# Performance work log

Measured on AMD Instinct MI355X. Metric: run time of the kernel, lower is better.

The kernel has to match this reference:

```python
import jax, jax.numpy as jnp
import numpy as np
from jax import lax

BN_EPS = 1e-5


def _conv1d(h, w, b=None):
    # h: [B, Cin, L], w: [Cout, Cin, K], 'same' padding for odd K
    k = w.shape[-1]
    out = lax.conv_general_dilated(h, w, (1,), [(k // 2, k // 2)],
                                   dimension_numbers=('NCH', 'OIH', 'NCH'))
    if b is not None:
        out = out + b[None, :, None]
    return out


def _bn(h, gamma, beta):
    # eval-mode BatchNorm1d with running_mean=0, running_var=1
    return h * (gamma[None, :, None] / jnp.sqrt(1.0 + BN_EPS)) + beta[None, :, None]


def _encoder(h, cw, cb, rw, gammas, betas, aw, au):
    # h: [B, D, L] -> V: [B, C, F]
    t = jnp.tanh(_conv1d(h, cw, cb))
    t = _bn(t, gammas[0], betas[0])
    for i in range(rw.shape[0]):  # residual blocks
        t = jnp.tanh(_bn(_conv1d(t, rw[i]), gammas[i + 1], betas[i + 1]) + t)
    # label attention: w [A,F], u [C,A]
    Z = jnp.tanh(jnp.einsum('af,bfl->bal', aw, t))
    A = jax.nn.softmax(jnp.einsum('ca,bal->bcl', au, Z), axis=2)
    V = jnp.einsum('bfl,bcl->bcf', t, A)
    return V


def setup_inputs() -> dict:
    key = jax.random.key(0)
    ks = list(jax.random.split(key, 32))
    B, L, D, C, VOC, NE, N, E = 16, 4096, 256, 50, 50000, 20050, 512, 8192
    F, A, FFN = 100, 256, 128

    def rn(k, shape, s):
        return (jax.random.normal(k, shape, jnp.float32) * s).astype(jnp.float32)

    x = jax.random.randint(ks[0], (B, L), 0, VOC)
    attention_mask = jnp.ones((B, L), jnp.int32)
    nodes = jax.random.randint(ks[1], (B, N), 0, NE)
    src = jax.random.randint(ks[2], (B, E), 0, N)
    off = jax.random.randint(ks[3], (B, E), 1, N)
    dst = (src + off) % N  # guaranteed no self-loops
    edges = jnp.stack([src, dst], axis=1)  # [B, 2, E]

    inp = dict(x=x, attention_mask=attention_mask, nodes=nodes, edges=edges)
    inp['word_emb'] = rn(ks[4], (VOC, D), 0.02)
    inp['entity_emb'] = rn(ks[5], (NE, D), 0.02)
    i = 6
    for ksz in (3, 5, 9):
        inp[f'convw{ksz}'] = rn(ks[i], (F, D, ksz), (2.0 / (D * ksz)) ** 0.5); i += 1
        inp[f'convb{ksz}'] = jnp.zeros((F,), jnp.float32)
        inp[f'resw{ksz}'] = rn(ks[i], (2, F, F, ksz), (2.0 / (F * ksz)) ** 0.5); i += 1
    inp['bn_gamma'] = jnp.ones((3, 3, F), jnp.float32)
    inp['bn_beta'] = jnp.zeros((3, 3, F), jnp.float32)
    inp['attn_w'] = rn(ks[i], (3, A, F), 0.05); i += 1
    inp['attn_u'] = rn(ks[i], (3, C, A), 0.05); i += 1
    inp['gc1_w'] = rn(ks[i], (D, D), (1.0 / D) ** 0.5); i += 1
    inp['gc1_b'] = jnp.zeros((D,), jnp.float32)
    inp['gc2_w'] = rn(ks[i], (D, D), (1.0 / D) ** 0.5); i += 1
    inp['gc2_b'] = jnp.zeros((D,), jnp.float32)
    inp['fin1_w'] = rn(ks[i], (FFN, 3 * F + D), 0.05); i += 1
    inp['fin1_b'] = jnp.zeros((FFN,), jnp.float32)
    inp['fin2_w'] = rn(ks[i], (C, FFN), 0.05); i += 1
    inp['fin2_b'] = jnp.zeros((C,), jnp.float32)
    return inp


def reference(x, attention_mask, nodes, edges, word_emb, entity_emb,
              convw3, convb3, resw3, convw5, convb5, resw5, convw9, convb9, resw9,
              bn_gamma, bn_beta, attn_w, attn_u,
              gc1_w, gc1_b, gc2_w, gc2_b, fin1_w, fin1_b, fin2_w, fin2_b):
    C = fin2_b.shape[0]
    h = word_emb[x]                      # [B, L, D]
    h = jnp.transpose(h, (0, 2, 1))      # [B, D, L]

    Vs = []
    for i, (cw, cb, rw) in enumerate([(convw3, convb3, resw3),
                                      (convw5, convb5, resw5),
                                      (convw9, convb9, resw9)]):
        Vs.append(_encoder(h, cw, cb, rw, bn_gamma[i], bn_beta[i], attn_w[i], attn_u[i]))
    V = jnp.concatenate(Vs, axis=2)      # [B, C, 300]

    node_emb = entity_emb[nodes]         # [B, N, D]

    def per_graph(ne, ei):
        N = ne.shape[0]
        sl = jnp.arange(N)
        s = jnp.concatenate([ei[0], sl])  # GCNConv adds self-loops
        d = jnp.concatenate([ei[1], sl])
        deg = jax.ops.segment_sum(jnp.ones(s.shape[0], jnp.float32), d, num_segments=N)
        dinv = jnp.where(deg > 0, lax.rsqrt(deg), 0.0)
        norm = (dinv[s] * dinv[d])[:, None]

        def gconv(hh, W, b):
            return jax.ops.segment_sum((hh @ W.T)[s] * norm, d, num_segments=N) + b

        g = jax.nn.relu(gconv(ne, gc1_w, gc1_b))
        g = gconv(g, gc2_w, gc2_b)
        return g[:C]

    out_graphs = jax.vmap(per_graph)(node_emb, edges)  # [B, C, D]

    out = jnp.concatenate([out_graphs, V], axis=2)     # [B, C, D+300]
    hid = jax.nn.relu(jnp.einsum('bcf,hf->bch', out, fin1_w) + fin1_b)
    y_hat = jnp.sum(fin2_w[None] * hid, axis=2) + fin2_b  # [B, C]
    return y_hat
```

## Files before the change

### kernel.cpp

```cpp
#include <hip/hip_runtime.h>


#define CDIV(a,b) (((a)+(b)-1)/(b))

#define B_    16
#define L_    4096
#define D_    256
#define LP_   4112
#define POFF  8
#define F_    100
#define A_    256
#define C_    50
#define NN_   512
#define EE_   8192
#define ADJ_  8704
#define OC_   560

#define WFC1_STRIDE ((size_t)9*8*8*512)
#define WFRES_STRIDE ((size_t)9*4*8*512)
#define WFAW_STRIDE ((size_t)4*16*512)
#define WFAU_STRIDE ((size_t)8*4*512)

typedef unsigned short u16;
using short8  = __attribute__((ext_vector_type(8))) short;
using short4v = __attribute__((ext_vector_type(4))) short;
using f32x4   = __attribute__((ext_vector_type(4))) float;

__device__ __forceinline__ u16 f2b(float f){
    unsigned u = __float_as_uint(f);
    u += 0x7FFF + ((u >> 16) & 1);
    return (u16)(u >> 16);
}
__device__ __forceinline__ float b2f(u16 h){ return __uint_as_float(((unsigned)h) << 16); }

__global__ void fill_i_k(int* p, int n, int v){
    int i = blockIdx.x*256 + threadIdx.x; if (i < n) p[i] = v;
}
__global__ void zero_pads1_k(u16* p){
    int idx = blockIdx.x*256 + threadIdx.x;
    if (idx >= B_*16*128) return;
    int ch = idx & 127; int rest = idx >> 7;
    int pc = rest & 15; int b = rest >> 4;
    int col = (pc < 8) ? pc : (4096 + pc);
    p[((size_t)b*LP_ + col)*128 + ch] = 0;
}

__global__ __launch_bounds__(256) void embed1_k(const int* __restrict__ x,
                                                const float* __restrict__ emb,
                                                u16* __restrict__ hH){
    int b = blockIdx.y;
    int col = blockIdx.x*8 + (threadIdx.x >> 5);
    int cg  = (threadIdx.x & 31) * 8;
    size_t o = ((size_t)b*LP_ + col)*D_ + cg;
    int l = col - POFF;
    short8 h0;
    if (l < 0 || l >= L_){
        #pragma unroll
        for (int i = 0; i < 8; ++i) h0[i] = 0;
    } else {
        int tok = x[b*L_ + l];
        const float* s = emb + (size_t)tok*D_ + cg;
        #pragma unroll
        for (int i = 0; i < 8; ++i) h0[i] = (short)f2b(s[i]);
    }
    *(short8*)(hH + o) = h0;
}

__device__ __forceinline__ void pack_frag(const float* src, u16* dst,
                                          int M, int K, int kt, int nch, int MTtot, int idx){
    int i = idx & 7, lane = (idx >> 3) & 63, rest = idx >> 9;
    int mt = rest % MTtot, r2 = rest / MTtot;
    int cc = r2 % nch,  j = r2 / nch;
    int m  = mt*16 + (lane & 15);
    int ch = cc*32 + (lane >> 4)*8 + i;
    float v = (m < M && ch < K) ? src[((size_t)m*K + ch)*kt + j] : 0.f;
    dst[(size_t)rest*512 + lane*8 + i] = f2b(v);
}
__global__ void pack_conv1_k(const float* w3, const float* w5, const float* w9, u16* dst){
    int br = blockIdx.y;
    int k = (br == 0) ? 3 : (br == 1) ? 5 : 9;
    const float* s = (br == 0) ? w3 : (br == 1) ? w5 : w9;
    int idx = blockIdx.x*256 + threadIdx.x;
    if (idx < k*8*8*512) pack_frag(s, dst + (size_t)br*WFC1_STRIDE, F_, 256, k, 8, 8, idx);
}
__global__ void pack_res_k(const float* w3, const float* w5, const float* w9, u16* dst){
    int br = blockIdx.y, blk = blockIdx.z;
    int k = (br == 0) ? 3 : (br == 1) ? 5 : 9;
    const float* s = ((br == 0) ? w3 : (br == 1) ? w5 : w9) + (size_t)blk*F_*F_*k;
    int idx = blockIdx.x*256 + threadIdx.x;
    if (idx < k*4*8*512) pack_frag(s, dst + (size_t)(br*2 + blk)*WFRES_STRIDE, F_, F_, k, 4, 8, idx);
}
__global__ void pack_aw_k(const float* aw, u16* dst){
    int br = blockIdx.y;
    int idx = blockIdx.x*256 + threadIdx.x;
    if (idx < 4*16*512) pack_frag(aw + (size_t)br*A_*F_, dst + (size_t)br*WFAW_STRIDE, A_, F_, 1, 4, 16, idx);
}
__global__ void pack_au_k(const float* au, u16* dst){
    int br = blockIdx.y;
    int idx = blockIdx.x*256 + threadIdx.x;
    if (idx < 8*4*512) pack_frag(au + (size_t)br*C_*A_, dst + (size_t)br*WFAU_STRIDE, C_, A_, 1, 8, 4, idx);
}
__global__ void transpose_fin1_k(const float* __restrict__ src, float* __restrict__ dst){
    int idx = blockIdx.x*256 + threadIdx.x;
    if (idx >= OC_*128) return;
    int h = idx & 127, j = idx >> 7;
    dst[idx] = (j < 556) ? src[h*556 + j] : 0.f;
}

template<int KT, int MODE>
__global__ __launch_bounds__(256) void conv_mfma_k(
    const u16* __restrict__ in, int CHp_in, int nch,
    const u16* __restrict__ wf,
    const float* __restrict__ bias, const float* __restrict__ gamma,
    const float* __restrict__ beta,
    u16* __restrict__ out, u16* __restrict__ outT)
{
    __shared__ short sm[4352];
    const int tid = threadIdx.x, lane = tid & 63;
    const int w = tid >> 6, wm = w >> 1, wn = w & 1;
    const int q = lane >> 4, lr = lane & 15;
    const int n0 = blockIdx.x * 64;
    const int b  = blockIdx.y;
    const u16* inb = in + (size_t)b*LP_*CHp_in;

    f32x4 acc[4][2];
    #pragma unroll
    for (int t = 0; t < 4; ++t)
        #pragma unroll
        for (int n = 0; n < 2; ++n) acc[t][n] = (f32x4){0.f,0.f,0.f,0.f};

    for (int cc = 0; cc < nch; ++cc){
        for (int idx = tid; idx < 320; idx += 256){
            int col = idx >> 2, qq = idx & 3;
            *(short8*)(sm + col*40 + qq*8) =
                *(const short8*)(inb + (size_t)(n0 + col)*CHp_in + cc*32 + qq*8);
        }
        __syncthreads();
        const u16* fpb = wf + (size_t)(cc*8 + wm*4)*512 + lane*8;
        short8 Ac[4];
        #pragma unroll
        for (int t = 0; t < 4; ++t) Ac[t] = *(const short8*)(fpb + (size_t)t*512);
        #pragma unroll
        for (int j = 0; j < KT; ++j){
            short8 An[4];
            if (j + 1 < KT){
                const u16* fn = fpb + (size_t)(j+1)*nch*8*512;
                #pragma unroll
                for (int t = 0; t < 4; ++t) An[t] = *(const short8*)(fn + (size_t)t*512);
            }
            int sc0 = 8 - (KT >> 1) + j + wn*32 + lr;
            short8 Bv[2];
            #pragma unroll
            for (int n = 0; n < 2; ++n)
                Bv[n] = *(const short8*)(sm + (sc0 + n*16)*40 + q*8);
            #pragma unroll
            for (int t = 0; t < 4; ++t)
                #pragma unroll
                for (int n = 0; n < 2; ++n)
                    acc[t][n] = __builtin_amdgcn_mfma_f32_16x16x32_bf16(Ac[t], Bv[n], acc[t][n], 0,0,0);
            if (j + 1 < KT){
                #pragma unroll
                for (int t = 0; t < 4; ++t) Ac[t] = An[t];
            }
        }
        __syncthreads();
    }

    const float BNS = 0.9999950000374997f;
    for (int p = 0; p < 2; ++p){
        if (wn == p){
            #pragma unroll
            for (int t = 0; t < 4; ++t){
                #pragma unroll
                for (int n = 0; n < 2; ++n){
                    int mbase = wm*64 + t*16 + q*4;
                    int cl = n*16 + lr;
                    int colg = n0 + p*32 + cl;
                    float rsum[4] = {0.f,0.f,0.f,0.f};
                    if (MODE == 1){
                        size_t ro = ((size_t)b*LP_ + POFF + colg)*CHp_in + mbase;
                        short4v rh = *(const short4v*)(in + ro);
                        #pragma unroll
                        for (int r = 0; r < 4; ++r) rsum[r] = b2f((u16)rh[r]);
                    }
                    short4v hv;
                    #pragma unroll
                    for (int r = 0; r < 4; ++r){
                        int mm = mbase + r;
                        float a = acc[t][n][r];
                        float v;
                        if (MODE == 0){
                            float bi=0.f, s=0.f, be=0.f;
                            if (mm < F_){ bi = bias[mm]; s = gamma[mm]*BNS; be = beta[mm]; }
                            v = tanhf(a + bi)*s + be;
                        } else {
                            float s=0.f, be=0.f;
                            if (mm < F_){ s = gamma[mm]*BNS; be = beta[mm]; }
                            v = tanhf(fmaf(a, s, be) + rsum[r]);
                        }
                        hv[r] = (short)f2b(v);
                    }
                    *(short4v*)(sm + cl*136 + mbase) = hv;
                }
            }
        }
        __syncthreads();
        for (int idx = tid; idx < 512; idx += 256){
            int col = idx >> 4, q8 = idx & 15;
            short8 vv = *(const short8*)(sm + col*136 + q8*8);
            *(short8*)(out + ((size_t)b*LP_ + POFF + n0 + p*32 + col)*128 + q8*8) = vv;
        }
        if (outT){
            int f = tid & 127, half = tid >> 7;
            u16 vals[16];
            #pragma unroll
            for (int i = 0; i < 16; ++i) vals[i] = (u16)sm[(half*16 + i)*136 + f];
            short8 v0, v1;
            #pragma unroll
            for (int i = 0; i < 8; ++i){ v0[i] = (short)vals[i]; v1[i] = (short)vals[8+i]; }
            u16* dst = outT + ((size_t)b*128 + f)*L_ + n0 + p*32 + half*16;
            *(short8*)dst = v0;
            *(short8*)(dst + 8) = v1;
        }
        __syncthreads();
    }
}

__global__ __launch_bounds__(256) void attn_k(const u16* __restrict__ tpl,
                                              const u16* __restrict__ awf,
                                              const u16* __restrict__ auf,
                                              float* __restrict__ S){
    __shared__ short sm[17408];
    const int tid = threadIdx.x, lane = tid & 63;
    const int w = tid >> 6, wm = w >> 1, wn = w & 1;
    const int q = lane >> 4, lr = lane & 15;
    const int n0 = blockIdx.x * 128;
    const int b  = blockIdx.y;

    for (int idx = tid; idx < 2048; idx += 256){
        int col = idx >> 4, g = idx & 15;
        *(short8*)(sm + col*136 + g*8) =
            *(const short8*)(tpl + ((size_t)b*LP_ + POFF + n0 + col)*128 + g*8);
    }
    __syncthreads();

    f32x4 acc1[8][4];
    #pragma unroll
    for (int t = 0; t < 8; ++t)
        #pragma unroll
        for (int n = 0; n < 4; ++n) acc1[t][n] = (f32x4){0.f,0.f,0.f,0.f};
    for (int cc = 0; cc < 4; ++cc){
        short8 Af[8];
        const u16* fp = awf + (size_t)(cc*16 + wm*8)*512 + lane*8;
        #pragma unroll
        for (int t = 0; t < 8; ++t) Af[t] = *(const short8*)(fp + (size_t)t*512);
        short8 Bf[4];
        #pragma unroll
        for (int n = 0; n < 4; ++n)
            Bf[n] = *(const short8*)(sm + (wn*64 + n*16 + lr)*136 + cc*32 + q*8);
        #pragma unroll
        for (int t = 0; t < 8; ++t)
            #pragma unroll
            for (int n = 0; n < 4; ++n)
                acc1[t][n] = __builtin_amdgcn_mfma_f32_16x16x32_bf16(Af[t], Bf[n], acc1[t][n], 0,0,0);
    }
    __syncthreads();

    for (int p = 0; p < 2; ++p){
        if (wn == p){
            #pragma unroll
            for (int t = 0; t < 8; ++t){
                #pragma unroll
                for (int n = 0; n < 4; ++n){
                    int abase = wm*128 + t*16 + q*4;
                    int cl = n*16 + lr;
                    short4v zv;
                    #pragma unroll
                    for (int r = 0; r < 4; ++r) zv[r] = (short)f2b(tanhf(acc1[t][n][r]));
                    *(short4v*)(sm + cl*264 + abase) = zv;
                }
            }
        }
        __syncthreads();
        f32x4 acc2[4];
        #pragma unroll
        for (int t = 0; t < 4; ++t) acc2[t] = (f32x4){0.f,0.f,0.f,0.f};
        for (int cc = 0; cc < 8; ++cc){
            short8 Af2[4];
            const u16* fp2 = auf + (size_t)(cc*4)*512 + lane*8;
            #pragma unroll
            for (int t = 0; t < 4; ++t) Af2[t] = *(const short8*)(fp2 + (size_t)t*512);
            short8 Bf2 = *(const short8*)(sm + (w*16 + lr)*264 + cc*32 + q*8);
            #pragma unroll
            for (int t = 0; t < 4; ++t)
                acc2[t] = __builtin_amdgcn_mfma_f32_16x16x32_bf16(Af2[t], Bf2, acc2[t], 0,0,0);
        }
        #pragma unroll
        for (int t = 0; t < 4; ++t)
            #pragma unroll
            for (int r = 0; r < 4; ++r){
                int c = t*16 + q*4 + r;
                S[((size_t)b*64 + c)*L_ + n0 + p*64 + w*16 + lr] = acc2[t][r];
            }
        __syncthreads();
    }
}

__global__ __launch_bounds__(256) void softmax_k(float* __restrict__ S){
    int c = blockIdx.x, b = blockIdx.y, t = threadIdx.x;
    float* p = S + ((size_t)b*64 + c)*L_;
    __shared__ float sh[256];
    float mx = -1e30f;
    for (int j = t; j < L_; j += 256) mx = fmaxf(mx, p[j]);
    sh[t] = mx; __syncthreads();
    for (int o = 128; o > 0; o >>= 1){ if (t < o) sh[t] = fmaxf(sh[t], sh[t+o]); __syncthreads(); }
    float m = sh[0]; __syncthreads();
    float sum = 0.f;
    for (int j = t; j < L_; j += 256){ float e = expf(p[j] - m); p[j] = e; sum += e; }
    sh[t] = sum; __syncthreads();
    for (int o = 128; o > 0; o >>= 1){ if (t < o) sh[t] += sh[t+o]; __syncthreads(); }
    float inv = 1.0f / sh[0];
    for (int j = t; j < L_; j += 256) p[j] *= inv;
}

__global__ __launch_bounds__(256) void v_mfma_k(const u16* __restrict__ tT,
                                                const float* __restrict__ S,
                                                float* __restrict__ Vpart){
    int cx = blockIdx.x, b = blockIdx.y;
    int w = threadIdx.x >> 6, lane = threadIdx.x & 63;
    int q = lane >> 4, lr = lane & 15;
    int l0 = cx*128;
    f32x4 acc[7];
    #pragma unroll
    for (int mt = 0; mt < 7; ++mt) acc[mt] = (f32x4){0.f,0.f,0.f,0.f};
    const u16* tb = tT + (size_t)b*128*L_;
    const float* Sb = S + ((size_t)b*64 + w*16 + lr)*L_;
    #pragma unroll
    for (int kk = 0; kk < 4; ++kk){
        int l = l0 + kk*32 + q*8;
        float4 s0 = *(const float4*)(Sb + l);
        float4 s1 = *(const float4*)(Sb + l + 4);
        short8 Bf;
        Bf[0] = (short)f2b(s0.x); Bf[1] = (short)f2b(s0.y);
        Bf[2] = (short)f2b(s0.z); Bf[3] = (short)f2b(s0.w);
        Bf[4] = (short)f2b(s1.x); Bf[5] = (short)f2b(s1.y);
        Bf[6] = (short)f2b(s1.z); Bf[7] = (short)f2b(s1.w);
        #pragma unroll
        for (int mt = 0; mt < 7; ++mt){
            short8 Af = *(const short8*)(tb + (size_t)(mt*16 + lr)*L_ + l);
            acc[mt] = __builtin_amdgcn_mfma_f32_16x16x32_bf16(Af, Bf, acc[mt], 0,0,0);
        }
    }
    int c = w*16 + lr;
    if (c < C_){
        float* vp = Vpart + ((size_t)(b*64 + c)*32 + cx)*112;
        #pragma unroll
        for (int mt = 0; mt < 7; ++mt)
            *(f32x4*)(vp + mt*16 + q*4) = acc[mt];
    }
}

__global__ void reduce_v_k(const float* __restrict__ Vp, float* __restrict__ oc, int coloff){
    int idx = blockIdx.x*256 + threadIdx.x;
    if (idx >= B_*C_*F_) return;
    int f = idx % F_; int rest = idx / F_;
    int c = rest % C_; int b = rest / C_;
    const float* src = Vp + ((size_t)(b*64 + c)*32)*112 + f;
    float s = 0.f;
    #pragma unroll
    for (int cx = 0; cx < 32; ++cx) s += src[cx*112];
    oc[((size_t)b*C_ + c)*OC_ + 256 + coloff + f] = s;
}

__global__ void gather_nodes_k(const int* __restrict__ nodes, const float* __restrict__ emb,
                               float* __restrict__ ne){
    int idx = blockIdx.x*256 + threadIdx.x;
    if (idx >= B_*NN_*D_) return;
    int d = idx & 255, n = (idx >> 8) & 511, b = idx >> 17;
    ne[idx] = emb[(size_t)nodes[b*NN_ + n]*D_ + d];
}
__global__ void deg_count_k(const int* __restrict__ edges, int* __restrict__ deg){
    int idx = blockIdx.x*256 + threadIdx.x;
    if (idx >= B_*EE_) return;
    int b = idx >> 13, e = idx & (EE_-1);
    int dst = edges[b*2*EE_ + EE_ + e];
    atomicAdd(&deg[b*NN_ + dst], 1);
}
__global__ void dinv_k(const int* __restrict__ deg, float* __restrict__ dinv){
    int i = blockIdx.x*256 + threadIdx.x;
    if (i < B_*NN_) dinv[i] = 1.0f / sqrtf((float)deg[i]);
}
__global__ void scan_csr_k(const int* __restrict__ deg, int* __restrict__ rp, int* __restrict__ cur){
    int b = blockIdx.x, t = threadIdx.x;
    __shared__ int sh[NN_];
    int v = deg[b*NN_ + t];
    sh[t] = v; __syncthreads();
    for (int off = 1; off < NN_; off <<= 1){
        int x = (t >= off) ? sh[t-off] : 0;
        __syncthreads();
        sh[t] += x;
        __syncthreads();
    }
    int incl = sh[t], excl = incl - v;
    rp[b*513 + t] = excl;
    cur[b*NN_ + t] = excl;
    if (t == NN_-1) rp[b*513 + NN_] = incl;
}
__global__ void fill_csr_k(const int* __restrict__ edges, int* __restrict__ cur, int* __restrict__ adj){
    int e = blockIdx.x*256 + threadIdx.x, b = blockIdx.y;
    if (e >= ADJ_) return;
    int s, d;
    if (e < EE_){ s = edges[b*2*EE_ + e]; d = edges[b*2*EE_ + EE_ + e]; }
    else        { s = d = e - EE_; }
    int pos = atomicAdd(&cur[b*NN_ + d], 1);
    adj[b*ADJ_ + pos] = s;
}
__global__ __launch_bounds__(256) void gemm_nt_k(const float* __restrict__ A,
                                                 const float* __restrict__ W,
                                                 float* __restrict__ out){
    int b = blockIdx.z, n0 = blockIdx.x*64, i0 = blockIdx.y*64;
    __shared__ float aL[64][17], wL[64][17];
    int tid = threadIdx.x, tx = tid & 15, ty = tid >> 4;
    const float* Ab = A + (size_t)b*NN_*D_;
    float acc[4][4];
    #pragma unroll
    for (int r = 0; r < 4; ++r)
        #pragma unroll
        for (int i = 0; i < 4; ++i) acc[r][i] = 0.f;
    for (int j0 = 0; j0 < D_; j0 += 16){
        for (int idx = tid; idx < 1024; idx += 256){
            int r = idx >> 4, cc = idx & 15;
            aL[r][cc] = Ab[(size_t)(n0+r)*D_ + j0 + cc];
            wL[r][cc] = W[(size_t)(i0+r)*D_ + j0 + cc];
        }
        __syncthreads();
        #pragma unroll
        for (int kk = 0; kk < 16; ++kk){
            float av[4], wv[4];
            #pragma unroll
            for (int r = 0; r < 4; ++r) av[r] = aL[ty*4+r][kk];
            #pragma unroll
            for (int i = 0; i < 4; ++i) wv[i] = wL[tx*4+i][kk];
            #pragma unroll
            for (int r = 0; r < 4; ++r)
                #pragma unroll
                for (int i = 0; i < 4; ++i) acc[r][i] = fmaf(av[r], wv[i], acc[r][i]);
        }
        __syncthreads();
    }
    float* ob = out + (size_t)b*NN_*D_;
    #pragma unroll
    for (int r = 0; r < 4; ++r)
        #pragma unroll
        for (int i = 0; i < 4; ++i)
            ob[(size_t)(n0+ty*4+r)*D_ + i0+tx*4+i] = acc[r][i];
}
__global__ __launch_bounds__(256) void scatter_k(const float* __restrict__ xw,
                                                 const int* __restrict__ adj,
                                                 const int* __restrict__ rp,
                                                 const float* __restrict__ dinv,
                                                 const float* __restrict__ bias,
                                                 float* __restrict__ out,
                                                 int out_bs, int out_ld, int relu){
    int n = blockIdx.x, b = blockIdx.y, t = threadIdx.x;
    const int* rpb = rp + b*513;
    const int* adjb = adj + b*ADJ_;
    const float* xwb = xw + (size_t)b*NN_*D_;
    const float* dvb = dinv + b*NN_;
    int e0 = rpb[n], e1 = rpb[n+1];
    float acc = 0.f;
    for (int e = e0; e < e1; ++e){
        int s = adjb[e];
        acc = fmaf(xwb[(size_t)s*D_ + t], dvb[s], acc);
    }
    float v = fmaf(acc, dvb[n], bias[t]);
    if (relu) v = fmaxf(v, 0.f);
    out[(size_t)b*out_bs + (size_t)n*out_ld + t] = v;
}

__global__ __launch_bounds__(128) void final_k(const float* __restrict__ oc,
                                               const float* __restrict__ w1t,
                                               const float* __restrict__ b1,
                                               const float* __restrict__ w2,
                                               const float* __restrict__ b2,
                                               float* __restrict__ y){
    int c = blockIdx.x, b = blockIdx.y, h = threadIdx.x;
    __shared__ float row[OC_];
    __shared__ float red[128];
    const float* src = oc + ((size_t)b*C_ + c)*OC_;
    for (int j = h; j < OC_; j += 128) row[j] = src[j];
    __syncthreads();
    float acc = b1[h];
    #pragma unroll 8
    for (int j = 0; j < OC_; ++j) acc = fmaf(row[j], w1t[j*128 + h], acc);
    float hid = fmaxf(acc, 0.f);
    red[h] = hid * w2[c*128 + h];
    __syncthreads();
    for (int o = 64; o > 0; o >>= 1){ if (h < o) red[h] += red[h+o]; __syncthreads(); }
    if (h == 0) y[b*C_ + c] = red[0] + b2[c];
}

extern "C" void kernel_launch(void* const* d_in, const int* in_sizes, int n_in,
                              void* d_out, int out_size, void* d_ws, size_t ws_size,
                              hipStream_t stream){
    (void)in_sizes; (void)n_in; (void)out_size; (void)ws_size;
    const int*   x          = (const int*)d_in[0];
    const int*   nodes      = (const int*)d_in[2];
    const int*   edges      = (const int*)d_in[3];
    const float* word_emb   = (const float*)d_in[4];
    const float* entity_emb = (const float*)d_in[5];
    const float* convb[3]   = {(const float*)d_in[7], (const float*)d_in[10], (const float*)d_in[13]};
    const float* bn_gamma   = (const float*)d_in[15];
    const float* bn_beta    = (const float*)d_in[16];
    const float* gc1_w      = (const float*)d_in[19];
    const float* gc1_b      = (const float*)d_in[20];
    const float* gc2_w      = (const float*)d_in[21];
    const float* gc2_b      = (const float*)d_in[22];
    const float* fin1_w     = (const float*)d_in[23];
    const float* fin1_b     = (const float*)d_in[24];
    const float* fin2_w     = (const float*)d_in[25];
    const float* fin2_b     = (const float*)d_in[26];
    float* y = (float*)d_out;

    char* base = (char*)d_ws;
    size_t off = 0;
    auto alloc = [&](size_t elems, size_t esz) -> char* {
        char* p = base + off;
        off += ((elems*esz + 255) / 256) * 256;
        return p;
    };
    u16* hH  = (u16*)alloc((size_t)B_*LP_*D_, 2);
    u16* t0  = (u16*)alloc((size_t)B_*LP_*128, 2);
    u16* t1  = (u16*)alloc((size_t)B_*LP_*128, 2);
    u16* tT  = (u16*)alloc((size_t)B_*128*L_, 2);
    float* S     = (float*)alloc((size_t)B_*64*L_, 4);
    float* Vpart = (float*)alloc((size_t)B_*64*32*112, 4);
    float* ne   = (float*)alloc((size_t)B_*NN_*D_, 4);
    float* xw   = (float*)alloc((size_t)B_*NN_*D_, 4);
    float* g1   = (float*)alloc((size_t)B_*NN_*D_, 4);
    float* ocat = (float*)alloc((size_t)B_*C_*OC_, 4);
    u16* wfc1  = (u16*)alloc(3*WFC1_STRIDE, 2);
    u16* wfres = (u16*)alloc(6*WFRES_STRIDE, 2);
    u16* wfaw  = (u16*)alloc(3*WFAW_STRIDE, 2);
    u16* wfau  = (u16*)alloc(3*WFAU_STRIDE, 2);
    float* w1t   = (float*)alloc((size_t)OC_*128, 4);
    float* dinvp = (float*)alloc((size_t)B_*NN_, 4);
    int* deg = (int*)alloc((size_t)B_*NN_, 4);
    int* rpB = (int*)alloc((size_t)B_*513, 4);
    int* cur = (int*)alloc((size_t)B_*NN_, 4);
    int* adj = (int*)alloc((size_t)B_*ADJ_, 4);

    fill_i_k<<<CDIV(B_*NN_,256),256,0,stream>>>(deg, B_*NN_, 1);
    zero_pads1_k<<<CDIV(B_*16*128,256),256,0,stream>>>(t0);
    zero_pads1_k<<<CDIV(B_*16*128,256),256,0,stream>>>(t1);
    pack_conv1_k<<<dim3(CDIV(9*8*8*512,256),3),256,0,stream>>>(
        (const float*)d_in[6], (const float*)d_in[9], (const float*)d_in[12], wfc1);
    pack_res_k<<<dim3(CDIV(9*4*8*512,256),3,2),256,0,stream>>>(
        (const float*)d_in[8], (const float*)d_in[11], (const float*)d_in[14], wfres);
    pack_aw_k<<<dim3(CDIV(4*16*512,256),3),256,0,stream>>>((const float*)d_in[17], wfaw);
    pack_au_k<<<dim3(CDIV(8*4*512,256),3),256,0,stream>>>((const float*)d_in[18], wfau);

    embed1_k<<<dim3(LP_/8, B_),256,0,stream>>>(x, word_emb, hH);

    gather_nodes_k<<<CDIV(B_*NN_*D_,256),256,0,stream>>>(nodes, entity_emb, ne);
    deg_count_k<<<CDIV(B_*EE_,256),256,0,stream>>>(edges, deg);
    dinv_k<<<CDIV(B_*NN_,256),256,0,stream>>>(deg, dinvp);
    scan_csr_k<<<B_,NN_,0,stream>>>(deg, rpB, cur);
    fill_csr_k<<<dim3(CDIV(ADJ_,256),B_),256,0,stream>>>(edges, cur, adj);
    gemm_nt_k<<<dim3(NN_/64, D_/64, B_),256,0,stream>>>(ne, gc1_w, xw);
    scatter_k<<<dim3(NN_,B_),256,0,stream>>>(xw, adj, rpB, dinvp, gc1_b, g1, NN_*D_, D_, 1);
    gemm_nt_k<<<dim3(NN_/64, D_/64, B_),256,0,stream>>>(g1, gc2_w, xw);
    scatter_k<<<dim3(C_,B_),256,0,stream>>>(xw, adj, rpB, dinvp, gc2_b, ocat, C_*OC_, OC_, 0);

    dim3 gc(64, B_), ga(32, B_);
    for (int br = 0; br < 3; ++br){
        const float* gam = bn_gamma + br*300;
        const float* bet = bn_beta + br*300;
        const u16* wc = wfc1 + (size_t)br*WFC1_STRIDE;
        const u16* wr1 = wfres + (size_t)(br*2+0)*WFRES_STRIDE;
        const u16* wr2 = wfres + (size_t)(br*2+1)*WFRES_STRIDE;
        if (br == 0){
            conv_mfma_k<3,0><<<gc,256,0,stream>>>(hH,256,8, wc, convb[br],gam,bet, t0, nullptr);
            conv_mfma_k<3,1><<<gc,256,0,stream>>>(t0,128,4, wr1, nullptr,gam+100,bet+100, t1, nullptr);
            conv_mfma_k<3,1><<<gc,256,0,stream>>>(t1,128,4, wr2, nullptr,gam+200,bet+200, t0, tT);
        } else if (br == 1){
            conv_mfma_k<5,0><<<gc,256,0,stream>>>(hH,256,8, wc, convb[br],gam,bet, t0, nullptr);
            conv_mfma_k<5,1><<<gc,256,0,stream>>>(t0,128,4, wr1, nullptr,gam+100,bet+100, t1, nullptr);
            conv_mfma_k<5,1><<<gc,256,0,stream>>>(t1,128,4, wr2, nullptr,gam+200,bet+200, t0, tT);
        } else {
            conv_mfma_k<9,0><<<gc,256,0,stream>>>(hH,256,8, wc, convb[br],gam,bet, t0, nullptr);
            conv_mfma_k<9,1><<<gc,256,0,stream>>>(t0,128,4, wr1, nullptr,gam+100,bet+100, t1, nullptr);
            conv_mfma_k<9,1><<<gc,256,0,stream>>>(t1,128,4, wr2, nullptr,gam+200,bet+200, t0, tT);
        }
        attn_k<<<ga,256,0,stream>>>(t0, wfaw + (size_t)br*WFAW_STRIDE,
                                    wfau + (size_t)br*WFAU_STRIDE, S);
        softmax_k<<<dim3(C_,B_),256,0,stream>>>(S);
        v_mfma_k<<<dim3(32, B_),256,0,stream>>>(tT, S, Vpart);
        reduce_v_k<<<CDIV(B_*C_*F_,256),256,0,stream>>>(Vpart, ocat, br*100);
    }

    transpose_fin1_k<<<CDIV(OC_*128,256),256,0,stream>>>(fin1_w, w1t);
    final_k<<<dim3(C_,B_),128,0,stream>>>(ocat, w1t, fin1_b, fin2_w, fin2_b, y);
}
```

Before: 858.0 us.

## Restructure conv MFMA kernel to stage four channel chunks per sync and retile warps

The conv kernel now loads four 32-channel chunks into shared memory per barrier pass instead of one, which cuts the number of __syncthreads round trips. The channel count becomes a template parameter so the loop fully unrolls. The warp tiling changes from a 2x2 (64 rows x 32 cols) split to each warp owning 32 output rows across all 64 columns, so each weight fragment load is reused across four B tiles. Shared memory grows to 12800 shorts per block, which may lower occupancy.

New measurement: 827.4 us. 1.04x faster.

```diff
diff --git a/kernel.cpp b/kernel.cpp
--- a/kernel.cpp
+++ b/kernel.cpp
@@ -107,101 +107,105 @@
     dst[idx] = (j < 556) ? src[h*556 + j] : 0.f;
 }
 
-template<int KT, int MODE>
+template<int KT, int MODE, int NCH>
 __global__ __launch_bounds__(256) void conv_mfma_k(
-    const u16* __restrict__ in, int CHp_in, int nch,
+    const u16* __restrict__ in, int CHp_in,
     const u16* __restrict__ wf,
     const float* __restrict__ bias, const float* __restrict__ gamma,
     const float* __restrict__ beta,
     u16* __restrict__ out, u16* __restrict__ outT)
 {
-    __shared__ short sm[4352];
+    __shared__ short sm[12800];
     const int tid = threadIdx.x, lane = tid & 63;
-    const int w = tid >> 6, wm = w >> 1, wn = w & 1;
+    const int w = tid >> 6;
     const int q = lane >> 4, lr = lane & 15;
     const int n0 = blockIdx.x * 64;
     const int b  = blockIdx.y;
     const u16* inb = in + (size_t)b*LP_*CHp_in;
 
-    f32x4 acc[4][2];
+    f32x4 acc[2][4];
     #pragma unroll
-    for (int t = 0; t < 4; ++t)
-        #pragma unroll
-        for (int n = 0; n < 2; ++n) acc[t][n] = (f32x4){0.f,0.f,0.f,0.f};
-
-    for (int cc = 0; cc < nch; ++cc){
-        for (int idx = tid; idx < 320; idx += 256){
-            int col = idx >> 2, qq = idx & 3;
-            *(short8*)(sm + col*40 + qq*8) =
-                *(const short8*)(inb + (size_t)(n0 + col)*CHp_in + cc*32 + qq*8);
-        }
-        __syncthreads();
-        const u16* fpb = wf + (size_t)(cc*8 + wm*4)*512 + lane*8;
-        short8 Ac[4];
-        #pragma unroll
-        for (int t = 0; t < 4; ++t) Ac[t] = *(const short8*)(fpb + (size_t)t*512);
-        #pragma unroll
-        for (int j = 0; j < KT; ++j){
-            short8 An[4];
-            if (j + 1 < KT){
-                const u16* fn = fpb + (size_t)(j+1)*nch*8*512;
-                #pragma unroll
-                for (int t = 0; t < 4; ++t) An[t] = *(const short8*)(fn + (size_t)t*512);
+    for (int t = 0; t < 2; ++t)
+        #pragma unroll
+        for (int n = 0; n < 4; ++n) acc[t][n] = (f32x4){0.f,0.f,0.f,0.f};
+
+    constexpr int NPASS = NCH / 4;
+    for (int pass = 0; pass < NPASS; ++pass){
+        for (int idx = tid; idx < 1280; idx += 256){
+            int cc = idx >> 8;
+            cc = idx / 320;
+            int e = idx - cc*320;
+            int col = e >> 2, qq = e & 3;
+            *(short8*)(sm + cc*3200 + col*40 + qq*8) =
+                *(const short8*)(inb + (size_t)(n0 + col)*CHp_in + (pass*4 + cc)*32 + qq*8);
+        }
+        __syncthreads();
+        auto fragPtr = [&](int it)->const u16*{
+            int j = it >> 2, cc = it & 3;
+            int rest = (j*NCH + pass*4 + cc)*8 + w*2;
+            return wf + (size_t)rest*512 + lane*8;
+        };
+        short8 Ac0 = *(const short8*)(fragPtr(0));
+        short8 Ac1 = *(const short8*)(fragPtr(0) + 512);
+        #pragma unroll
+        for (int it = 0; it < KT*4; ++it){
+            short8 An0, An1;
+            if (it + 1 < KT*4){
+                const u16* fn = fragPtr(it+1);
+                An0 = *(const short8*)(fn);
+                An1 = *(const short8*)(fn + 512);
             }
-            int sc0 = 8 - (KT >> 1) + j + wn*32 + lr;
-            short8 Bv[2];
-            #pragma unroll
-            for (int n = 0; n < 2; ++n)
-                Bv[n] = *(const short8*)(sm + (sc0 + n*16)*40 + q*8);
-            #pragma unroll
-            for (int t = 0; t < 4; ++t)
-                #pragma unroll
-                for (int n = 0; n < 2; ++n)
-                    acc[t][n] = __builtin_amdgcn_mfma_f32_16x16x32_bf16(Ac[t], Bv[n], acc[t][n], 0,0,0);
-            if (j + 1 < KT){
-                #pragma unroll
-                for (int t = 0; t < 4; ++t) Ac[t] = An[t];
+            int j = it >> 2, cc = it & 3;
+            int sc0 = 8 - (KT >> 1) + j + lr;
+            short8 Bv[4];
+            #pragma unroll
+            for (int n = 0; n < 4; ++n)
+                Bv[n] = *(const short8*)(sm + cc*3200 + (sc0 + n*16)*40 + q*8);
+            #pragma unroll
+            for (int n = 0; n < 4; ++n){
+                acc[0][n] = __builtin_amdgcn_mfma_f32_16x16x32_bf16(Ac0, Bv[n], acc[0][n], 0,0,0);
+                acc[1][n] = __builtin_amdgcn_mfma_f32_16x16x32_bf16(Ac1, Bv[n], acc[1][n], 0,0,0);
             }
+            if (it + 1 < KT*4){ Ac0 = An0; Ac1 = An1; }
         }
         __syncthreads();
     }
 
     const float BNS = 0.9999950000374997f;
     for (int p = 0; p < 2; ++p){
-        if (wn == p){
-            #pragma unroll
-            for (int t = 0; t < 4; ++t){
+        #pragma unroll
+        for (int t = 0; t < 2; ++t){
+            #pragma unroll
+            for (int u = 0; u < 2; ++u){
+                int n = p*2 + u;
+                int mbase = w*32 + t*16 + q*4;
+                int cl = u*16 + lr;
+                int colg = n0 + n*16 + lr;
+                float rsum[4] = {0.f,0.f,0.f,0.f};
+                if (MODE == 1){
+                    size_t ro = ((size_t)b*LP_ + POFF + colg)*CHp_in + mbase;
+                    short4v rh = *(const short4v*)(in + ro);
+                    #pragma unroll
+                    for (int r = 0; r < 4; ++r) rsum[r] = b2f((u16)rh[r]);
+                }
+                short4v hv;
                 #pragma unroll
-                for (int n = 0; n < 2; ++n){
-                    int mbase = wm*64 + t*16 + q*4;
-                    int cl = n*16 + lr;
-                    int colg = n0 + p*32 + cl;
-                    float rsum[4] = {0.f,0.f,0.f,0.f};
-                    if (MODE == 1){
-                        size_t ro = ((size_t)b*LP_ + POFF + colg)*CHp_in + mbase;
-                        short4v rh = *(const short4v*)(in + ro);
-                        #pragma unroll
-                        for (int r = 0; r < 4; ++r) rsum[r] = b2f((u16)rh[r]);
+                for (int r = 0; r < 4; ++r){
+                    int mm = mbase + r;
+                    float a = acc[t][n][r];
+                    float v;
+                    if (MODE == 0){
+                        float bi=0.f, s=0.f, be=0.f;
+                        if (mm < F_){ bi = bias[mm]; s = gamma[mm]*BNS; be = beta[mm]; }
+                        v = tanhf(a + bi)*s + be;
+                    } else {
+                        float s=0.f, be=0.f;
+                        if (mm < F_){ s = gamma[mm]*BNS; be = beta[mm]; }
+                        v = tanhf(fmaf(a, s, be) + rsum[r]);
                     }
-                    short4v hv;
-                    #pragma unroll
-                    for (int r = 0; r < 4; ++r){
-                        int mm = mbase + r;
-                        float a = acc[t][n][r];
-                        float v;
-                        if (MODE == 0){
-                            float bi=0.f, s=0.f, be=0.f;
-                            if (mm < F_){ bi = bias[mm]; s = gamma[mm]*BNS; be = beta[mm]; }
-                            v = tanhf(a + bi)*s + be;
-                        } else {
-                            float s=0.f, be=0.f;
-                            if (mm < F_){ s = gamma[mm]*BNS; be = beta[mm]; }
-                            v = tanhf(fmaf(a, s, be) + rsum[r]);
-                        }
-                        hv[r] = (short)f2b(v);
-                    }
-                    *(short4v*)(sm + cl*136 + mbase) = hv;
+                    hv[r] = (short)f2b(v);
                 }
+                *(short4v*)(sm + cl*136 + mbase) = hv;
             }
         }
         __syncthreads();
@@ -580,17 +584,17 @@
         const u16* wr1 = wfres + (size_t)(br*2+0)*WFRES_STRIDE;
         const u16* wr2 = wfres + (size_t)(br*2+1)*WFRES_STRIDE;
         if (br == 0){
-            conv_mfma_k<3,0><<<gc,256,0,stream>>>(hH,256,8, wc, convb[br],gam,bet, t0, nullptr);
-            conv_mfma_k<3,1><<<gc,256,0,stream>>>(t0,128,4, wr1, nullptr,gam+100,bet+100, t1, nullptr);
-            conv_mfma_k<3,1><<<gc,256,0,stream>>>(t1,128,4, wr2, nullptr,gam+200,bet+200, t0, tT);
+            conv_mfma_k<3,0,8><<<gc,256,0,stream>>>(hH,256, wc, convb[br],gam,bet, t0, nullptr);
+            conv_mfma_k<3,1,4><<<gc,256,0,stream>>>(t0,128, wr1, nullptr,gam+100,bet+100, t1, nullptr);
+            conv_mfma_k<3,1,4><<<gc,256,0,stream>>>(t1,128, wr2, nullptr,gam+200,bet+200, t0, tT);
         } else if (br == 1){
-            conv_mfma_k<5,0><<<gc,256,0,stream>>>(hH,256,8, wc, convb[br],gam,bet, t0, nullptr);
-            conv_mfma_k<5,1><<<gc,256,0,stream>>>(t0,128,4, wr1, nullptr,gam+100,bet+100, t1, nullptr);
-            conv_mfma_k<5,1><<<gc,256,0,stream>>>(t1,128,4, wr2, nullptr,gam+200,bet+200, t0, tT);
+            conv_mfma_k<5,0,8><<<gc,256,0,stream>>>(hH,256, wc, convb[br],gam,bet, t0, nullptr);
+            conv_mfma_k<5,1,4><<<gc,256,0,stream>>>(t0,128, wr1, nullptr,gam+100,bet+100, t1, nullptr);
+            conv_mfma_k<5,1,4><<<gc,256,0,stream>>>(t1,128, wr2, nullptr,gam+200,bet+200, t0, tT);
         } else {
-            conv_mfma_k<9,0><<<gc,256,0,stream>>>(hH,256,8, wc, convb[br],gam,bet, t0, nullptr);
-            conv_mfma_k<9,1><<<gc,256,0,stream>>>(t0,128,4, wr1, nullptr,gam+100,bet+100, t1, nullptr);
-            conv_mfma_k<9,1><<<gc,256,0,stream>>>(t1,128,4, wr2, nullptr,gam+200,bet+200, t0, tT);
+            conv_mfma_k<9,0,8><<<gc,256,0,stream>>>(hH,256, wc, convb[br],gam,bet, t0, nullptr);
+            conv_mfma_k<9,1,4><<<gc,256,0,stream>>>(t0,128, wr1, nullptr,gam+100,bet+100, t1, nullptr);
+            conv_mfma_k<9,1,4><<<gc,256,0,stream>>>(t1,128, wr2, nullptr,gam+200,bet+200, t0, tT);
         }
         attn_k<<<ga,256,0,stream>>>(t0, wfaw + (size_t)br*WFAW_STRIDE,
                                     wfau + (size_t)br*WFAU_STRIDE, S);
```
